# Performance work log

Hardware: AMD Instinct MI355X
Metric: run time of the kernel (lower is better)

Reference implementation:

```python
import jax, jax.numpy as jnp
import numpy as np

B, T, C, H = 512, 40, 512, 512


def _gru_dir(x, Wih, Whh, bih, bhh):
    """Single-direction PyTorch-convention GRU. x: [B,T,C] -> [B,T,H]."""
    Hh = Whh.shape[1]
    # precompute input projections for all timesteps: [B,T,3H]
    gx = jnp.einsum('btc,gc->btg', x, Wih) + bih

    def step(h, gxt):
        gh = h @ Whh.T + bhh  # [B,3H]
        r = jax.nn.sigmoid(gxt[:, :Hh] + gh[:, :Hh])
        z = jax.nn.sigmoid(gxt[:, Hh:2 * Hh] + gh[:, Hh:2 * Hh])
        n = jnp.tanh(gxt[:, 2 * Hh:] + r * gh[:, 2 * Hh:])
        h_new = (1.0 - z) * n + z * h
        return h_new, h_new

    h0 = jnp.zeros((x.shape[0], Hh), x.dtype)
    _, ys = jax.lax.scan(step, h0, jnp.swapaxes(gx, 0, 1))  # [T,B,H]
    return jnp.swapaxes(ys, 0, 1)


def setup_inputs() -> dict:
    key = jax.random.key(0)
    ks = jax.random.split(key, 10)
    s = 1.0 / np.sqrt(H)  # PyTorch default init scale
    lengths = jax.random.randint(ks[0], (B,), 5, T + 1)
    valid = jnp.arange(T)[None, :] < lengths[:, None]  # [B,T]
    ref_expr = jax.random.normal(ks[1], (B, T, C), jnp.float32) * valid[..., None]
    mk = lambda k, shape: jax.random.uniform(k, shape, jnp.float32, -s, s)
    return {
        'ref_expr': ref_expr,
        'Wih_f': mk(ks[2], (3 * H, C)), 'Whh_f': mk(ks[3], (3 * H, H)),
        'bih_f': mk(ks[4], (3 * H,)), 'bhh_f': mk(ks[5], (3 * H,)),
        'Wih_b': mk(ks[6], (3 * H, C)), 'Whh_b': mk(ks[7], (3 * H, H)),
        'bih_b': mk(ks[8], (3 * H,)), 'bhh_b': mk(ks[9], (3 * H,)),
    }


def reference(ref_expr, Wih_f, Whh_f, bih_f, bhh_f, Wih_b, Whh_b, bih_b, bhh_b):
    # padded positions are all-zero embedding vectors -> masked out
    valid = jnp.any(ref_expr != 0, axis=-1)  # [B,T], True = keep
    y_fwd = _gru_dir(ref_expr, Wih_f, Whh_f, bih_f, bhh_f)
    y_bwd = _gru_dir(ref_expr[:, ::-1], Wih_b, Whh_b, bih_b, bhh_b)[:, ::-1]
    y_word = jnp.concatenate([y_fwd, y_bwd], axis=-1)  # [B,T,2H]
    # masked max pooling over valid tokens (output_type='max')
    neg = jnp.finfo(y_word.dtype).min
    y = jnp.max(jnp.where(valid[..., None], y_word, neg), axis=1, keepdims=True)
    return y  # [B,1,2H]
```

## Files before the change

kernel.cpp:

```cpp
#include <hip/hip_runtime.h>
#include <hip/hip_bf16.h>
#include <float.h>

#define BB 512
#define TT 40
#define CC 512
#define HH 512

typedef short bf16x8 __attribute__((ext_vector_type(8)));
typedef float f32x4 __attribute__((ext_vector_type(4)));
typedef unsigned short ushortx8 __attribute__((ext_vector_type(8)));

__device__ __forceinline__ unsigned short f2bf(float f){
  union { float f; unsigned int i; } v; v.f = f;
  unsigned int r = v.i + 0x7fffu + ((v.i >> 16) & 1u);
  return (unsigned short)(r >> 16);
}

__device__ __forceinline__ bf16x8 load_sc0(const unsigned short* p){
  bf16x8 r;
  asm volatile("global_load_dwordx4 %0, %1, off sc0" : "=v"(r) : "v"(p));
  return r;
}
#define WAITV(N) do { asm volatile("s_waitcnt vmcnt(" #N ")" ::: "memory"); \
                      __builtin_amdgcn_sched_barrier(0); } while(0)

__device__ __forceinline__ float fast_sigmoid(float x){
  return __builtin_amdgcn_rcpf(1.f + __expf(-x));
}
__device__ __forceinline__ float fast_tanh(float x){
  return 1.f - 2.f*__builtin_amdgcn_rcpf(__expf(2.f*x) + 1.f);
}

__global__ void prep_x_kernel(const float* __restrict__ x, unsigned short* __restrict__ xb,
                              float* __restrict__ maskT){
  int w = blockIdx.x*4 + (threadIdx.x>>6);
  int lane = threadIdx.x & 63;
  const float* src = x + (size_t)w*CC + lane*8;
  f32x4 a = *(const f32x4*)(src);
  f32x4 b = *(const f32x4*)(src+4);
  ushortx8 o;
  o[0]=f2bf(a[0]); o[1]=f2bf(a[1]); o[2]=f2bf(a[2]); o[3]=f2bf(a[3]);
  o[4]=f2bf(b[0]); o[5]=f2bf(b[1]); o[6]=f2bf(b[2]); o[7]=f2bf(b[3]);
  *(ushortx8*)(xb + (size_t)w*CC + lane*8) = o;
  bool nz = (a[0]!=0.f)||(a[1]!=0.f)||(a[2]!=0.f)||(a[3]!=0.f)||
            (b[0]!=0.f)||(b[1]!=0.f)||(b[2]!=0.f)||(b[3]!=0.f);
  unsigned long long bal = __ballot(nz);
  if (lane==0){
    int b_ = w / TT, t_ = w % TT;
    maskT[t_*BB + b_] = bal ? 1.0f : 0.0f;
  }
}

__global__ void cvt_kernel(const float* __restrict__ src, unsigned short* __restrict__ dst, int n){
  int i = blockIdx.x*blockDim.x + threadIdx.x;
  if (i < n) dst[i] = f2bf(src[i]);
}

__global__ void init_h_kernel(unsigned short* __restrict__ hb, unsigned int* __restrict__ ctr){
  int i = blockIdx.x*blockDim.x + threadIdx.x;
  hb[i] = 0;
  if (i < 8) ctr[i*32] = 0u;
}

__global__ __launch_bounds__(256) void gru_persist_kernel(
    const unsigned short* __restrict__ xb,
    const unsigned short* __restrict__ wihF, const unsigned short* __restrict__ whhF,
    const unsigned short* __restrict__ wihB, const unsigned short* __restrict__ whhB,
    const float* __restrict__ bihF, const float* __restrict__ bhhF,
    const float* __restrict__ bihB, const float* __restrict__ bhhB,
    const float* __restrict__ maskT,
    unsigned short* __restrict__ hb,
    float* __restrict__ out, unsigned int* __restrict__ ctr)
{
  const int bid   = blockIdx.x;
  const int grp   = bid & 7;
  const int strip = bid >> 3;
  const int dir   = grp >> 2;
  const int bslab = grp & 3;
  const int b0 = bslab * 128;
  const int n0 = strip * 16;
  unsigned int* myctr = ctr + grp*32;

  const unsigned short* wih = dir ? wihB : wihF;
  const unsigned short* whh = dir ? whhB : whhF;
  const float* bih = dir ? bihB : bihF;
  const float* bhh = dir ? bhhB : bhhF;

  const int tid  = threadIdx.x;
  const int lane = tid & 63;
  const int lr   = lane & 15;
  const int lkg  = lane >> 4;
  const int wv   = tid >> 6;
  const int wrow = wv * 32;

  __shared__ __align__(16) unsigned short wlds[48 * 1024];
  for (int q = tid; q < 6144; q += 256) {
    const int row = q >> 7;
    const int kc  = (q & 127) * 8;
    const int g   = row >> 4;
    const int c   = row & 15;
    const unsigned short* src =
        (kc < 512 ? wih : whh) + ((size_t)(g*HH + n0 + c))*512 + (kc & 511);
    const int kb = kc * 2;
    *(ushortx8*)((char*)wlds + row*2048 + (kb ^ ((row & 7) << 4))) =
        *(const ushortx8*)src;
  }
  __syncthreads();

  const int jj = n0 + lr;
  const float br  = bih[jj]        + bhh[jj];
  const float bz  = bih[HH + jj]   + bhh[HH + jj];
  const float bnx = bih[2*HH + jj];
  const float bnh = bhh[2*HH + jj];

  float omax[2][4], hreg[2][4];
  #pragma unroll
  for (int mf=0; mf<2; ++mf)
    #pragma unroll
    for (int j=0; j<4; ++j){ omax[mf][j] = -FLT_MAX; hreg[mf][j] = 0.f; }

  const int swz = (lr & 7) << 4;
  const char* wbase = (const char*)wlds + lr*2048;

  for (int t = 0; t < TT; ++t) {
    const int tx = dir ? (TT-1-t) : t;
    const int bi = t & 1;
    const unsigned short* hbin = hb + (size_t)(dir*2 + bi)      * (BB*HH);
    unsigned short* hbout      = hb + (size_t)(dir*2 + (bi^1))  * (BB*HH);

    f32x4 ar[2], az[2], anx[2], anh[2];
    #pragma unroll
    for (int mf=0; mf<2; ++mf){ ar[mf]=0.f; az[mf]=0.f; anx[mf]=0.f; anh[mf]=0.f; }

    const unsigned short* xr0 = xb + ((size_t)(b0 + wrow + lr     )*TT + tx)*CC;
    const unsigned short* xr1 = xb + ((size_t)(b0 + wrow + 16 + lr)*TT + tx)*CC;

    #pragma unroll
    for (int kk = 0; kk < 16; ++kk) {
      const int ko = kk*32 + lkg*8;
      bf16x8 a0 = *(const bf16x8*)(xr0 + ko);
      bf16x8 a1 = *(const bf16x8*)(xr1 + ko);
      const int kbx = (ko*2) ^ swz;
      bf16x8 brf = *(const bf16x8*)(wbase +         kbx);
      bf16x8 bzf = *(const bf16x8*)(wbase + 32768 + kbx);
      bf16x8 bnf = *(const bf16x8*)(wbase + 65536 + kbx);
      ar[0]  = __builtin_amdgcn_mfma_f32_16x16x32_bf16(a0, brf, ar[0],0,0,0);
      ar[1]  = __builtin_amdgcn_mfma_f32_16x16x32_bf16(a1, brf, ar[1],0,0,0);
      az[0]  = __builtin_amdgcn_mfma_f32_16x16x32_bf16(a0, bzf, az[0],0,0,0);
      az[1]  = __builtin_amdgcn_mfma_f32_16x16x32_bf16(a1, bzf, az[1],0,0,0);
      anx[0] = __builtin_amdgcn_mfma_f32_16x16x32_bf16(a0, bnf, anx[0],0,0,0);
      anx[1] = __builtin_amdgcn_mfma_f32_16x16x32_bf16(a1, bnf, anx[1],0,0,0);
    }

    const float* mrow = maskT + tx*BB + b0 + wrow + lkg*4;
    const f32x4 mk0 = *(const f32x4*)(mrow);
    const f32x4 mk1 = *(const f32x4*)(mrow + 16);

    if (t > 0) {
      const unsigned int tgt = 128u*(unsigned)t;
      unsigned int spin = 0;
      while (__hip_atomic_load(myctr, __ATOMIC_RELAXED, __HIP_MEMORY_SCOPE_AGENT) < tgt
             && ++spin < (1u<<24))
        __builtin_amdgcn_s_sleep(1);
    }

    WAITV(0);

    const unsigned short* hr0 = hbin + (size_t)(b0 + wrow + lr     )*HH;
    const unsigned short* hr1 = hbin + (size_t)(b0 + wrow + 16 + lr)*HH;
    bf16x8 c0 = load_sc0(hr0 + lkg*8);
    bf16x8 c1 = load_sc0(hr1 + lkg*8);
    #pragma unroll
    for (int kk = 0; kk < 16; ++kk) {
      const int ko = kk*32 + lkg*8;
      bf16x8 p0, p1;
      if (kk < 15) { p0 = load_sc0(hr0 + ko + 32); p1 = load_sc0(hr1 + ko + 32); }
      const int kbx = (1024 + ko*2) ^ swz;
      bf16x8 brf = *(const bf16x8*)(wbase +         kbx);
      bf16x8 bzf = *(const bf16x8*)(wbase + 32768 + kbx);
      bf16x8 bnf = *(const bf16x8*)(wbase + 65536 + kbx);
      if (kk < 15) { WAITV(2); } else { WAITV(0); }
      ar[0]  = __builtin_amdgcn_mfma_f32_16x16x32_bf16(c0, brf, ar[0],0,0,0);
      ar[1]  = __builtin_amdgcn_mfma_f32_16x16x32_bf16(c1, brf, ar[1],0,0,0);
      az[0]  = __builtin_amdgcn_mfma_f32_16x16x32_bf16(c0, bzf, az[0],0,0,0);
      az[1]  = __builtin_amdgcn_mfma_f32_16x16x32_bf16(c1, bzf, az[1],0,0,0);
      anh[0] = __builtin_amdgcn_mfma_f32_16x16x32_bf16(c0, bnf, anh[0],0,0,0);
      anh[1] = __builtin_amdgcn_mfma_f32_16x16x32_bf16(c1, bnf, anh[1],0,0,0);
      if (kk < 15) { c0 = p0; c1 = p1; }
    }

    #pragma unroll
    for (int mf=0; mf<2; ++mf){
      const f32x4 mk = mf ? mk1 : mk0;
      #pragma unroll
      for (int j=0; j<4; ++j){
        const int m = wrow + mf*16 + lkg*4 + j;
        const int b = b0 + m;
        const float rg = fast_sigmoid(ar[mf][j] + br);
        const float zg = fast_sigmoid(az[mf][j] + bz);
        const float ng = fast_tanh(anx[mf][j] + bnx + rg*(anh[mf][j] + bnh));
        const float hn = (1.f - zg)*ng + zg*hreg[mf][j];
        hreg[mf][j] = hn;
        hbout[(size_t)b*HH + jj] = f2bf(hn);
        const float cand = (mk[j] != 0.f) ? hn : -FLT_MAX;
        omax[mf][j] = fmaxf(omax[mf][j], cand);
      }
    }

    if (t < TT-1) {
      WAITV(0);
      if (lane == 0)
        __hip_atomic_fetch_add(myctr, 1u, __ATOMIC_RELAXED, __HIP_MEMORY_SCOPE_AGENT);
    }
  }

  #pragma unroll
  for (int mf=0; mf<2; ++mf){
    #pragma unroll
    for (int j=0; j<4; ++j){
      const int b = b0 + wrow + mf*16 + lkg*4 + j;
      out[(size_t)b*(2*HH) + dir*HH + jj] = omax[mf][j];
    }
  }
}

extern "C" void kernel_launch(void* const* d_in, const int* in_sizes, int n_in,
                              void* d_out, int out_size, void* d_ws, size_t ws_size,
                              hipStream_t stream) {
  const float* x    = (const float*)d_in[0];
  const float* WihF = (const float*)d_in[1];
  const float* WhhF = (const float*)d_in[2];
  const float* bihF = (const float*)d_in[3];
  const float* bhhF = (const float*)d_in[4];
  const float* WihB = (const float*)d_in[5];
  const float* WhhB = (const float*)d_in[6];
  const float* bihB = (const float*)d_in[7];
  const float* bhhB = (const float*)d_in[8];
  float* out = (float*)d_out;

  char* ws = (char*)d_ws;
  unsigned short* xb    = (unsigned short*)(ws);
  unsigned short* wb    = (unsigned short*)(ws + 20971520);
  unsigned short* wihFb = wb;
  unsigned short* whhFb = wb + 786432;
  unsigned short* wihBb = wb + 2*786432;
  unsigned short* whhBb = wb + 3*786432;
  float* maskT = (float*)(ws + 27262976);
  unsigned short* hb = (unsigned short*)(ws + 27344896);
  unsigned int* ctr  = (unsigned int*)(ws + 29442048);

  prep_x_kernel<<<BB*TT/4, 256, 0, stream>>>(x, xb, maskT);
  cvt_kernel<<<3072, 256, 0, stream>>>(WihF, wihFb, 786432);
  cvt_kernel<<<3072, 256, 0, stream>>>(WhhF, whhFb, 786432);
  cvt_kernel<<<3072, 256, 0, stream>>>(WihB, wihBb, 786432);
  cvt_kernel<<<3072, 256, 0, stream>>>(WhhB, whhBb, 786432);
  init_h_kernel<<<4096, 256, 0, stream>>>(hb, ctr);

  gru_persist_kernel<<<256, 256, 0, stream>>>(xb, wihFb, whhFb, wihBb, whhBb,
                                              bihF, bhhF, bihB, bhhB,
                                              maskT, hb, out, ctr);
}
```

Before: 355.7 us.

## Split GRU block into producer and consumer waves for input and recurrent GEMMs

Each workgroup now has 512 threads. Four producer waves compute the input-projection MFMAs for upcoming timesteps and pass the partial gate accumulators through double-buffered LDS slots, using workgroup-scope flag handshakes. Four consumer waves handle only the recurrent h·Whh GEMM, the gate nonlinearities and the cross-block synchronisation. The goal is to take the x·Wih work off the serial recurrence critical path. The cost is extra LDS traffic, intra-block spin-waits and higher LDS usage (about 148 KB), which must still fit one block per CU.

New measurement: 917.8 us. 158% more time.

```diff
diff --git a/kernel.cpp b/kernel.cpp
--- a/kernel.cpp
+++ b/kernel.cpp
@@ -10,6 +10,11 @@
 typedef short bf16x8 __attribute__((ext_vector_type(8)));
 typedef float f32x4 __attribute__((ext_vector_type(4)));
 typedef unsigned short ushortx8 __attribute__((ext_vector_type(8)));
+
+#define LDSH 49152
+#define LDSA 98304
+#define LDSF 147456
+#define LDSTOT 147968
 
 __device__ __forceinline__ unsigned short f2bf(float f){
   union { float f; unsigned int i; } v; v.f = f;
@@ -63,7 +68,7 @@
   if (i < 8) ctr[i*32] = 0u;
 }
 
-__global__ __launch_bounds__(256) void gru_persist_kernel(
+__global__ __launch_bounds__(512, 2) void gru_persist_kernel(
     const unsigned short* __restrict__ xb,
     const unsigned short* __restrict__ wihF, const unsigned short* __restrict__ whhF,
     const unsigned short* __restrict__ wihB, const unsigned short* __restrict__ whhB,
@@ -92,136 +97,194 @@
   const int lr   = lane & 15;
   const int lkg  = lane >> 4;
   const int wv   = tid >> 6;
-  const int wrow = wv * 32;
-
-  __shared__ __align__(16) unsigned short wlds[48 * 1024];
-  for (int q = tid; q < 6144; q += 256) {
-    const int row = q >> 7;
-    const int kc  = (q & 127) * 8;
-    const int g   = row >> 4;
-    const int c   = row & 15;
+
+  __shared__ __align__(16) char smem[LDSTOT];
+
+  for (int q = tid; q < 6144; q += 512) {
+    const int p_  = q >= 3072;
+    const int r_  = p_ ? (q - 3072) : q;
+    const int row = r_ >> 6;
+    const int kc  = (r_ & 63) * 8;
     const unsigned short* src =
-        (kc < 512 ? wih : whh) + ((size_t)(g*HH + n0 + c))*512 + (kc & 511);
-    const int kb = kc * 2;
-    *(ushortx8*)((char*)wlds + row*2048 + (kb ^ ((row & 7) << 4))) =
+        (p_ ? whh : wih) + ((size_t)((row>>4)*HH + n0 + (row&15)))*512 + kc;
+    *(ushortx8*)(smem + p_*LDSH + row*1024 + ((kc*2) ^ ((row&15)<<4))) =
         *(const ushortx8*)src;
   }
+  if (tid < 4)      *(unsigned int*)(smem + LDSF + tid*16) = 0u;
+  else if (tid < 8) *(unsigned int*)(smem + LDSF + 256 + (tid-4)*16) = 0u;
   __syncthreads();
 
-  const int jj = n0 + lr;
-  const float br  = bih[jj]        + bhh[jj];
-  const float bz  = bih[HH + jj]   + bhh[HH + jj];
-  const float bnx = bih[2*HH + jj];
-  const float bnh = bhh[2*HH + jj];
-
-  float omax[2][4], hreg[2][4];
-  #pragma unroll
-  for (int mf=0; mf<2; ++mf)
+  const int swz = lr << 4;
+
+  if (wv < 4) {
+    const int pair = wv;
+    const int wrow = pair * 32;
+    unsigned int* prod = (unsigned int*)(smem + LDSF + pair*16);
+    unsigned int* cons = (unsigned int*)(smem + LDSF + 256 + pair*16);
+    const char* wb_ = smem + lr*1024;
+
+    for (int t = 0; t < TT; ++t) {
+      const int tx = dir ? (TT-1-t) : t;
+      f32x4 ar[2], az[2], anx[2];
+      #pragma unroll
+      for (int mf=0; mf<2; ++mf){ ar[mf]=0.f; az[mf]=0.f; anx[mf]=0.f; }
+
+      const unsigned short* xr0 = xb + ((size_t)(b0 + wrow + lr     )*TT + tx)*CC;
+      const unsigned short* xr1 = xb + ((size_t)(b0 + wrow + 16 + lr)*TT + tx)*CC;
+
+      #pragma unroll
+      for (int kk = 0; kk < 16; ++kk) {
+        const int ko = kk*32 + lkg*8;
+        bf16x8 a0 = *(const bf16x8*)(xr0 + ko);
+        bf16x8 a1 = *(const bf16x8*)(xr1 + ko);
+        const int kbx = (ko*2) ^ swz;
+        bf16x8 brf = *(const bf16x8*)(wb_ +         kbx);
+        bf16x8 bzf = *(const bf16x8*)(wb_ + 16384 + kbx);
+        bf16x8 bnf = *(const bf16x8*)(wb_ + 32768 + kbx);
+        ar[0]  = __builtin_amdgcn_mfma_f32_16x16x32_bf16(a0, brf, ar[0],0,0,0);
+        ar[1]  = __builtin_amdgcn_mfma_f32_16x16x32_bf16(a1, brf, ar[1],0,0,0);
+        az[0]  = __builtin_amdgcn_mfma_f32_16x16x32_bf16(a0, bzf, az[0],0,0,0);
+        az[1]  = __builtin_amdgcn_mfma_f32_16x16x32_bf16(a1, bzf, az[1],0,0,0);
+        anx[0] = __builtin_amdgcn_mfma_f32_16x16x32_bf16(a0, bnf, anx[0],0,0,0);
+        anx[1] = __builtin_amdgcn_mfma_f32_16x16x32_bf16(a1, bnf, anx[1],0,0,0);
+      }
+
+      if (t >= 2) {
+        const unsigned int tgt = (unsigned)(t-1);
+        unsigned int spin = 0;
+        while (__hip_atomic_load(cons, __ATOMIC_ACQUIRE, __HIP_MEMORY_SCOPE_WORKGROUP) < tgt
+               && ++spin < (1u<<24))
+          __builtin_amdgcn_s_sleep(1);
+      }
+
+      char* slot = smem + LDSA + (pair*2 + (t&1))*6144 + lane*16;
+      *(f32x4*)(slot + 0*1024) = ar[0];
+      *(f32x4*)(slot + 1*1024) = ar[1];
+      *(f32x4*)(slot + 2*1024) = az[0];
+      *(f32x4*)(slot + 3*1024) = az[1];
+      *(f32x4*)(slot + 4*1024) = anx[0];
+      *(f32x4*)(slot + 5*1024) = anx[1];
+      if (lane == 0)
+        __hip_atomic_fetch_add(prod, 1u, __ATOMIC_RELEASE, __HIP_MEMORY_SCOPE_WORKGROUP);
+    }
+  } else {
+    const int pair = wv - 4;
+    const int wrow = pair * 32;
+    unsigned int* prod = (unsigned int*)(smem + LDSF + pair*16);
+    unsigned int* cons = (unsigned int*)(smem + LDSF + 256 + pair*16);
+    const char* wb_ = smem + LDSH + lr*1024;
+
+    const int jj = n0 + lr;
+    const float br  = bih[jj]        + bhh[jj];
+    const float bz  = bih[HH + jj]   + bhh[HH + jj];
+    const float bnx = bih[2*HH + jj];
+    const float bnh = bhh[2*HH + jj];
+
+    float omax[2][4], hreg[2][4];
     #pragma unroll
-    for (int j=0; j<4; ++j){ omax[mf][j] = -FLT_MAX; hreg[mf][j] = 0.f; }
-
-  const int swz = (lr & 7) << 4;
-  const char* wbase = (const char*)wlds + lr*2048;
-
-  for (int t = 0; t < TT; ++t) {
-    const int tx = dir ? (TT-1-t) : t;
-    const int bi = t & 1;
-    const unsigned short* hbin = hb + (size_t)(dir*2 + bi)      * (BB*HH);
-    unsigned short* hbout      = hb + (size_t)(dir*2 + (bi^1))  * (BB*HH);
-
-    f32x4 ar[2], az[2], anx[2], anh[2];
+    for (int mf=0; mf<2; ++mf)
+      #pragma unroll
+      for (int j=0; j<4; ++j){ omax[mf][j] = -FLT_MAX; hreg[mf][j] = 0.f; }
+
+    for (int t = 0; t < TT; ++t) {
+      const int tx = dir ? (TT-1-t) : t;
+      const int bi = t & 1;
+      const unsigned short* hbin = hb + (size_t)(dir*2 + bi)      * (BB*HH);
+      unsigned short* hbout      = hb + (size_t)(dir*2 + (bi^1))  * (BB*HH);
+
+      f32x4 ar[2], az[2], anh[2];
+      #pragma unroll
+      for (int mf=0; mf<2; ++mf){ ar[mf]=0.f; az[mf]=0.f; anh[mf]=0.f; }
+
+      const float* mrow = maskT + tx*BB + b0 + wrow + lkg*4;
+      const f32x4 mk0 = *(const f32x4*)(mrow);
+      const f32x4 mk1 = *(const f32x4*)(mrow + 16);
+
+      if (t > 0) {
+        const unsigned int tgt = 128u*(unsigned)t;
+        unsigned int spin = 0;
+        while (__hip_atomic_load(myctr, __ATOMIC_RELAXED, __HIP_MEMORY_SCOPE_AGENT) < tgt
+               && ++spin < (1u<<24))
+          __builtin_amdgcn_s_sleep(1);
+      }
+      WAITV(0);
+
+      const unsigned short* hr0 = hbin + (size_t)(b0 + wrow + lr     )*HH;
+      const unsigned short* hr1 = hbin + (size_t)(b0 + wrow + 16 + lr)*HH;
+      bf16x8 c0 = load_sc0(hr0 + lkg*8);
+      bf16x8 c1 = load_sc0(hr1 + lkg*8);
+      #pragma unroll
+      for (int kk = 0; kk < 16; ++kk) {
+        const int ko = kk*32 + lkg*8;
+        bf16x8 p0, p1;
+        if (kk < 15) { p0 = load_sc0(hr0 + ko + 32); p1 = load_sc0(hr1 + ko + 32); }
+        const int kbx = (ko*2) ^ swz;
+        bf16x8 brf = *(const bf16x8*)(wb_ +         kbx);
+        bf16x8 bzf = *(const bf16x8*)(wb_ + 16384 + kbx);
+        bf16x8 bnf = *(const bf16x8*)(wb_ + 32768 + kbx);
+        if (kk < 15) { WAITV(2); } else { WAITV(0); }
+        ar[0]  = __builtin_amdgcn_mfma_f32_16x16x32_bf16(c0, brf, ar[0],0,0,0);
+        ar[1]  = __builtin_amdgcn_mfma_f32_16x16x32_bf16(c1, brf, ar[1],0,0,0);
+        az[0]  = __builtin_amdgcn_mfma_f32_16x16x32_bf16(c0, bzf, az[0],0,0,0);
+        az[1]  = __builtin_amdgcn_mfma_f32_16x16x32_bf16(c1, bzf, az[1],0,0,0);
+        anh[0] = __builtin_amdgcn_mfma_f32_16x16x32_bf16(c0, bnf, anh[0],0,0,0);
+        anh[1] = __builtin_amdgcn_mfma_f32_16x16x32_bf16(c1, bnf, anh[1],0,0,0);
+        if (kk < 15) { c0 = p0; c1 = p1; }
+      }
+
+      {
+        unsigned int spin = 0;
+        const unsigned int tgt = (unsigned)(t+1);
+        while (__hip_atomic_load(prod, __ATOMIC_ACQUIRE, __HIP_MEMORY_SCOPE_WORKGROUP) < tgt
+               && ++spin < (1u<<24))
+          __builtin_amdgcn_s_sleep(1);
+      }
+      const char* slot = smem + LDSA + (pair*2 + (t&1))*6144 + lane*16;
+      f32x4 px0 = *(const f32x4*)(slot + 0*1024);
+      f32x4 px1 = *(const f32x4*)(slot + 1*1024);
+      f32x4 pz0 = *(const f32x4*)(slot + 2*1024);
+      f32x4 pz1 = *(const f32x4*)(slot + 3*1024);
+      f32x4 pn0 = *(const f32x4*)(slot + 4*1024);
+      f32x4 pn1 = *(const f32x4*)(slot + 5*1024);
+      asm volatile("s_waitcnt lgkmcnt(0)" ::: "memory");
+      if (lane == 0)
+        __hip_atomic_fetch_add(cons, 1u, __ATOMIC_RELEASE, __HIP_MEMORY_SCOPE_WORKGROUP);
+      ar[0] += px0; ar[1] += px1;
+      az[0] += pz0; az[1] += pz1;
+      const f32x4 anx0 = pn0, anx1 = pn1;
+
+      #pragma unroll
+      for (int mf=0; mf<2; ++mf){
+        const f32x4 mk = mf ? mk1 : mk0;
+        const f32x4 anx_ = mf ? anx1 : anx0;
+        #pragma unroll
+        for (int j=0; j<4; ++j){
+          const int b = b0 + wrow + mf*16 + lkg*4 + j;
+          const float rg = fast_sigmoid(ar[mf][j] + br);
+          const float zg = fast_sigmoid(az[mf][j] + bz);
+          const float ng = fast_tanh(anx_[j] + bnx + rg*(anh[mf][j] + bnh));
+          const float hn = (1.f - zg)*ng + zg*hreg[mf][j];
+          hreg[mf][j] = hn;
+          hbout[(size_t)b*HH + jj] = f2bf(hn);
+          const float cand = (mk[j] != 0.f) ? hn : -FLT_MAX;
+          omax[mf][j] = fmaxf(omax[mf][j], cand);
+        }
+      }
+
+      if (t < TT-1) {
+        WAITV(0);
+        if (lane == 0)
+          __hip_atomic_fetch_add(myctr, 1u, __ATOMIC_RELAXED, __HIP_MEMORY_SCOPE_AGENT);
+      }
+    }
+
     #pragma unroll
-    for (int mf=0; mf<2; ++mf){ ar[mf]=0.f; az[mf]=0.f; anx[mf]=0.f; anh[mf]=0.f; }
-
-    const unsigned short* xr0 = xb + ((size_t)(b0 + wrow + lr     )*TT + tx)*CC;
-    const unsigned short* xr1 = xb + ((size_t)(b0 + wrow + 16 + lr)*TT + tx)*CC;
-
-    #pragma unroll
-    for (int kk = 0; kk < 16; ++kk) {
-      const int ko = kk*32 + lkg*8;
-      bf16x8 a0 = *(const bf16x8*)(xr0 + ko);
-      bf16x8 a1 = *(const bf16x8*)(xr1 + ko);
-      const int kbx = (ko*2) ^ swz;
-      bf16x8 brf = *(const bf16x8*)(wbase +         kbx);
-      bf16x8 bzf = *(const bf16x8*)(wbase + 32768 + kbx);
-      bf16x8 bnf = *(const bf16x8*)(wbase + 65536 + kbx);
-      ar[0]  = __builtin_amdgcn_mfma_f32_16x16x32_bf16(a0, brf, ar[0],0,0,0);
-      ar[1]  = __builtin_amdgcn_mfma_f32_16x16x32_bf16(a1, brf, ar[1],0,0,0);
-      az[0]  = __builtin_amdgcn_mfma_f32_16x16x32_bf16(a0, bzf, az[0],0,0,0);
-      az[1]  = __builtin_amdgcn_mfma_f32_16x16x32_bf16(a1, bzf, az[1],0,0,0);
-      anx[0] = __builtin_amdgcn_mfma_f32_16x16x32_bf16(a0, bnf, anx[0],0,0,0);
-      anx[1] = __builtin_amdgcn_mfma_f32_16x16x32_bf16(a1, bnf, anx[1],0,0,0);
-    }
-
-    const float* mrow = maskT + tx*BB + b0 + wrow + lkg*4;
-    const f32x4 mk0 = *(const f32x4*)(mrow);
-    const f32x4 mk1 = *(const f32x4*)(mrow + 16);
-
-    if (t > 0) {
-      const unsigned int tgt = 128u*(unsigned)t;
-      unsigned int spin = 0;
-      while (__hip_atomic_load(myctr, __ATOMIC_RELAXED, __HIP_MEMORY_SCOPE_AGENT) < tgt
-             && ++spin < (1u<<24))
-        __builtin_amdgcn_s_sleep(1);
-    }
-
-    WAITV(0);
-
-    const unsigned short* hr0 = hbin + (size_t)(b0 + wrow + lr     )*HH;
-    const unsigned short* hr1 = hbin + (size_t)(b0 + wrow + 16 + lr)*HH;
-    bf16x8 c0 = load_sc0(hr0 + lkg*8);
-    bf16x8 c1 = load_sc0(hr1 + lkg*8);
-    #pragma unroll
-    for (int kk = 0; kk < 16; ++kk) {
-      const int ko = kk*32 + lkg*8;
-      bf16x8 p0, p1;
-      if (kk < 15) { p0 = load_sc0(hr0 + ko + 32); p1 = load_sc0(hr1 + ko + 32); }
-      const int kbx = (1024 + ko*2) ^ swz;
-      bf16x8 brf = *(const bf16x8*)(wbase +         kbx);
-      bf16x8 bzf = *(const bf16x8*)(wbase + 32768 + kbx);
-      bf16x8 bnf = *(const bf16x8*)(wbase + 65536 + kbx);
-      if (kk < 15) { WAITV(2); } else { WAITV(0); }
-      ar[0]  = __builtin_amdgcn_mfma_f32_16x16x32_bf16(c0, brf, ar[0],0,0,0);
-      ar[1]  = __builtin_amdgcn_mfma_f32_16x16x32_bf16(c1, brf, ar[1],0,0,0);
-      az[0]  = __builtin_amdgcn_mfma_f32_16x16x32_bf16(c0, bzf, az[0],0,0,0);
-      az[1]  = __builtin_amdgcn_mfma_f32_16x16x32_bf16(c1, bzf, az[1],0,0,0);
-      anh[0] = __builtin_amdgcn_mfma_f32_16x16x32_bf16(c0, bnf, anh[0],0,0,0);
-      anh[1] = __builtin_amdgcn_mfma_f32_16x16x32_bf16(c1, bnf, anh[1],0,0,0);
-      if (kk < 15) { c0 = p0; c1 = p1; }
-    }
-
-    #pragma unroll
-    for (int mf=0; mf<2; ++mf){
-      const f32x4 mk = mf ? mk1 : mk0;
+    for (int mf=0; mf<2; ++mf)
       #pragma unroll
       for (int j=0; j<4; ++j){
-        const int m = wrow + mf*16 + lkg*4 + j;
-        const int b = b0 + m;
-        const float rg = fast_sigmoid(ar[mf][j] + br);
-        const float zg = fast_sigmoid(az[mf][j] + bz);
-        const float ng = fast_tanh(anx[mf][j] + bnx + rg*(anh[mf][j] + bnh));
-        const float hn = (1.f - zg)*ng + zg*hreg[mf][j];
-        hreg[mf][j] = hn;
-        hbout[(size_t)b*HH + jj] = f2bf(hn);
-        const float cand = (mk[j] != 0.f) ? hn : -FLT_MAX;
-        omax[mf][j] = fmaxf(omax[mf][j], cand);
-      }
-    }
-
-    if (t < TT-1) {
-      WAITV(0);
-      if (lane == 0)
-        __hip_atomic_fetch_add(myctr, 1u, __ATOMIC_RELAXED, __HIP_MEMORY_SCOPE_AGENT);
-    }
-  }
-
-  #pragma unroll
-  for (int mf=0; mf<2; ++mf){
-    #pragma unroll
-    for (int j=0; j<4; ++j){
-      const int b = b0 + wrow + mf*16 + lkg*4 + j;
-      out[(size_t)b*(2*HH) + dir*HH + jj] = omax[mf][j];
-    }
+        const int b = b0 + wrow + mf*16 + lkg*4 + j;
+        out[(size_t)b*(2*HH) + dir*HH + (n0 + lr)] = omax[mf][j];
+      }
   }
 }
 
@@ -257,7 +320,7 @@
   cvt_kernel<<<3072, 256, 0, stream>>>(WhhB, whhBb, 786432);
   init_h_kernel<<<4096, 256, 0, stream>>>(hb, ctr);
 
-  gru_persist_kernel<<<256, 256, 0, stream>>>(xb, wihFb, whhFb, wihBb, whhBb,
+  gru_persist_kernel<<<256, 512, 0, stream>>>(xb, wihFb, whhFb, wihBb, whhBb,
                                               bihF, bhhF, bihB, bhhB,
                                               maskT, hb, out, ctr);
 }
```

## Hierarchical block barrier, deeper h prefetch, split LDS layout, vectorized weight convert

Applied to the files above, without the earlier changes.

Each workgroup now gathers its four waves in a shared-memory arrive counter and has a single lane increment the global per-group counter. One lane also polls that global counter and releases the others through an LDS flag, which cuts global atomic traffic and polling contention. The hidden-state loads use a four-deep register prefetch ring instead of double buffering. The weights are split into separate input and hidden LDS halves with a new swizzle, and the bf16 conversion kernels now process 8 elements per thread. The intra-block handoff adds an extra serialization step and uses more registers.

Result: slower. 370.9 us (+4.3%).

```diff
diff --git a/kernel.cpp b/kernel.cpp
--- a/kernel.cpp
+++ b/kernel.cpp
@@ -10,6 +10,10 @@
 typedef short bf16x8 __attribute__((ext_vector_type(8)));
 typedef float f32x4 __attribute__((ext_vector_type(4)));
 typedef unsigned short ushortx8 __attribute__((ext_vector_type(8)));
+
+#define LDSH 49152
+#define LDSF 98304
+#define LDSTOT 98320
 
 __device__ __forceinline__ unsigned short f2bf(float f){
   union { float f; unsigned int i; } v; v.f = f;
@@ -52,9 +56,16 @@
   }
 }
 
-__global__ void cvt_kernel(const float* __restrict__ src, unsigned short* __restrict__ dst, int n){
+__global__ void cvt_kernel(const float* __restrict__ src, unsigned short* __restrict__ dst, int n8){
   int i = blockIdx.x*blockDim.x + threadIdx.x;
-  if (i < n) dst[i] = f2bf(src[i]);
+  if (i < n8){
+    f32x4 a = *(const f32x4*)(src + i*8);
+    f32x4 b = *(const f32x4*)(src + i*8 + 4);
+    ushortx8 o;
+    o[0]=f2bf(a[0]); o[1]=f2bf(a[1]); o[2]=f2bf(a[2]); o[3]=f2bf(a[3]);
+    o[4]=f2bf(b[0]); o[5]=f2bf(b[1]); o[6]=f2bf(b[2]); o[7]=f2bf(b[3]);
+    *(ushortx8*)(dst + i*8) = o;
+  }
 }
 
 __global__ void init_h_kernel(unsigned short* __restrict__ hb, unsigned int* __restrict__ ctr){
@@ -94,18 +105,21 @@
   const int wv   = tid >> 6;
   const int wrow = wv * 32;
 
-  __shared__ __align__(16) unsigned short wlds[48 * 1024];
+  __shared__ __align__(16) char smem[LDSTOT];
+  unsigned int* arrive = (unsigned int*)(smem + LDSF);
+  unsigned int* goflag = (unsigned int*)(smem + LDSF + 8);
+
   for (int q = tid; q < 6144; q += 256) {
-    const int row = q >> 7;
-    const int kc  = (q & 127) * 8;
-    const int g   = row >> 4;
-    const int c   = row & 15;
+    const int p_  = q >= 3072;
+    const int r_  = p_ ? (q - 3072) : q;
+    const int row = r_ >> 6;
+    const int kc  = (r_ & 63) * 8;
     const unsigned short* src =
-        (kc < 512 ? wih : whh) + ((size_t)(g*HH + n0 + c))*512 + (kc & 511);
-    const int kb = kc * 2;
-    *(ushortx8*)((char*)wlds + row*2048 + (kb ^ ((row & 7) << 4))) =
+        (p_ ? whh : wih) + ((size_t)((row>>4)*HH + n0 + (row&15)))*512 + kc;
+    *(ushortx8*)(smem + p_*LDSH + row*1024 + ((kc*2) ^ ((row&15)<<4))) =
         *(const ushortx8*)src;
   }
+  if (tid == 0){ arrive[0] = 0u; goflag[0] = 0u; }
   __syncthreads();
 
   const int jj = n0 + lr;
@@ -120,8 +134,9 @@
     #pragma unroll
     for (int j=0; j<4; ++j){ omax[mf][j] = -FLT_MAX; hreg[mf][j] = 0.f; }
 
-  const int swz = (lr & 7) << 4;
-  const char* wbase = (const char*)wlds + lr*2048;
+  const int swz = lr << 4;
+  const char* wbx = smem + lr*1024;
+  const char* wbh = smem + LDSH + lr*1024;
 
   for (int t = 0; t < TT; ++t) {
     const int tx = dir ? (TT-1-t) : t;
@@ -142,9 +157,9 @@
       bf16x8 a0 = *(const bf16x8*)(xr0 + ko);
       bf16x8 a1 = *(const bf16x8*)(xr1 + ko);
       const int kbx = (ko*2) ^ swz;
-      bf16x8 brf = *(const bf16x8*)(wbase +         kbx);
-      bf16x8 bzf = *(const bf16x8*)(wbase + 32768 + kbx);
-      bf16x8 bnf = *(const bf16x8*)(wbase + 65536 + kbx);
+      bf16x8 brf = *(const bf16x8*)(wbx +         kbx);
+      bf16x8 bzf = *(const bf16x8*)(wbx + 16384 + kbx);
+      bf16x8 bnf = *(const bf16x8*)(wbx + 32768 + kbx);
       ar[0]  = __builtin_amdgcn_mfma_f32_16x16x32_bf16(a0, brf, ar[0],0,0,0);
       ar[1]  = __builtin_amdgcn_mfma_f32_16x16x32_bf16(a1, brf, ar[1],0,0,0);
       az[0]  = __builtin_amdgcn_mfma_f32_16x16x32_bf16(a0, bzf, az[0],0,0,0);
@@ -158,9 +173,16 @@
     const f32x4 mk1 = *(const f32x4*)(mrow + 16);
 
     if (t > 0) {
-      const unsigned int tgt = 128u*(unsigned)t;
+      if (wv == 0 && lane == 0) {
+        const unsigned int tgt = 32u*(unsigned)t;
+        unsigned int spin = 0;
+        while (__hip_atomic_load(myctr, __ATOMIC_RELAXED, __HIP_MEMORY_SCOPE_AGENT) < tgt
+               && ++spin < (1u<<24))
+          __builtin_amdgcn_s_sleep(2);
+        __hip_atomic_store(goflag, (unsigned)t, __ATOMIC_RELEASE, __HIP_MEMORY_SCOPE_WORKGROUP);
+      }
       unsigned int spin = 0;
-      while (__hip_atomic_load(myctr, __ATOMIC_RELAXED, __HIP_MEMORY_SCOPE_AGENT) < tgt
+      while (__hip_atomic_load(goflag, __ATOMIC_ACQUIRE, __HIP_MEMORY_SCOPE_WORKGROUP) < (unsigned)t
              && ++spin < (1u<<24))
         __builtin_amdgcn_s_sleep(1);
     }
@@ -169,25 +191,35 @@
 
     const unsigned short* hr0 = hbin + (size_t)(b0 + wrow + lr     )*HH;
     const unsigned short* hr1 = hbin + (size_t)(b0 + wrow + 16 + lr)*HH;
-    bf16x8 c0 = load_sc0(hr0 + lkg*8);
-    bf16x8 c1 = load_sc0(hr1 + lkg*8);
+    bf16x8 ph[4][2];
+    #pragma unroll
+    for (int q = 0; q < 4; ++q){
+      ph[q][0] = load_sc0(hr0 + q*32 + lkg*8);
+      ph[q][1] = load_sc0(hr1 + q*32 + lkg*8);
+    }
     #pragma unroll
     for (int kk = 0; kk < 16; ++kk) {
       const int ko = kk*32 + lkg*8;
-      bf16x8 p0, p1;
-      if (kk < 15) { p0 = load_sc0(hr0 + ko + 32); p1 = load_sc0(hr1 + ko + 32); }
-      const int kbx = (1024 + ko*2) ^ swz;
-      bf16x8 brf = *(const bf16x8*)(wbase +         kbx);
-      bf16x8 bzf = *(const bf16x8*)(wbase + 32768 + kbx);
-      bf16x8 bnf = *(const bf16x8*)(wbase + 65536 + kbx);
-      if (kk < 15) { WAITV(2); } else { WAITV(0); }
+      const int kbx = (ko*2) ^ swz;
+      bf16x8 brf = *(const bf16x8*)(wbh +         kbx);
+      bf16x8 bzf = *(const bf16x8*)(wbh + 16384 + kbx);
+      bf16x8 bnf = *(const bf16x8*)(wbh + 32768 + kbx);
+      if (kk < 13)      { WAITV(6); }
+      else if (kk == 13){ WAITV(4); }
+      else if (kk == 14){ WAITV(2); }
+      else              { WAITV(0); }
+      bf16x8 c0 = ph[kk&3][0];
+      bf16x8 c1 = ph[kk&3][1];
       ar[0]  = __builtin_amdgcn_mfma_f32_16x16x32_bf16(c0, brf, ar[0],0,0,0);
       ar[1]  = __builtin_amdgcn_mfma_f32_16x16x32_bf16(c1, brf, ar[1],0,0,0);
       az[0]  = __builtin_amdgcn_mfma_f32_16x16x32_bf16(c0, bzf, az[0],0,0,0);
       az[1]  = __builtin_amdgcn_mfma_f32_16x16x32_bf16(c1, bzf, az[1],0,0,0);
       anh[0] = __builtin_amdgcn_mfma_f32_16x16x32_bf16(c0, bnf, anh[0],0,0,0);
       anh[1] = __builtin_amdgcn_mfma_f32_16x16x32_bf16(c1, bnf, anh[1],0,0,0);
-      if (kk < 15) { c0 = p0; c1 = p1; }
+      if (kk < 12) {
+        ph[kk&3][0] = load_sc0(hr0 + (kk+4)*32 + lkg*8);
+        ph[kk&3][1] = load_sc0(hr1 + (kk+4)*32 + lkg*8);
+      }
     }
 
     #pragma unroll
@@ -195,8 +227,7 @@
       const f32x4 mk = mf ? mk1 : mk0;
       #pragma unroll
       for (int j=0; j<4; ++j){
-        const int m = wrow + mf*16 + lkg*4 + j;
-        const int b = b0 + m;
+        const int b = b0 + wrow + mf*16 + lkg*4 + j;
         const float rg = fast_sigmoid(ar[mf][j] + br);
         const float zg = fast_sigmoid(az[mf][j] + bz);
         const float ng = fast_tanh(anx[mf][j] + bnx + rg*(anh[mf][j] + bnh));
@@ -211,18 +242,25 @@
     if (t < TT-1) {
       WAITV(0);
       if (lane == 0)
+        __hip_atomic_fetch_add(arrive, 1u, __ATOMIC_RELEASE, __HIP_MEMORY_SCOPE_WORKGROUP);
+      if (wv == 0 && lane == 0) {
+        const unsigned int tgt = 4u*(unsigned)(t+1);
+        unsigned int spin = 0;
+        while (__hip_atomic_load(arrive, __ATOMIC_ACQUIRE, __HIP_MEMORY_SCOPE_WORKGROUP) < tgt
+               && ++spin < (1u<<24))
+          __builtin_amdgcn_s_sleep(1);
         __hip_atomic_fetch_add(myctr, 1u, __ATOMIC_RELAXED, __HIP_MEMORY_SCOPE_AGENT);
+      }
     }
   }
 
   #pragma unroll
-  for (int mf=0; mf<2; ++mf){
+  for (int mf=0; mf<2; ++mf)
     #pragma unroll
     for (int j=0; j<4; ++j){
       const int b = b0 + wrow + mf*16 + lkg*4 + j;
       out[(size_t)b*(2*HH) + dir*HH + jj] = omax[mf][j];
     }
-  }
 }
 
 extern "C" void kernel_launch(void* const* d_in, const int* in_sizes, int n_in,
@@ -251,10 +289,10 @@
   unsigned int* ctr  = (unsigned int*)(ws + 29442048);
 
   prep_x_kernel<<<BB*TT/4, 256, 0, stream>>>(x, xb, maskT);
-  cvt_kernel<<<3072, 256, 0, stream>>>(WihF, wihFb, 786432);
-  cvt_kernel<<<3072, 256, 0, stream>>>(WhhF, whhFb, 786432);
-  cvt_kernel<<<3072, 256, 0, stream>>>(WihB, wihBb, 786432);
-  cvt_kernel<<<3072, 256, 0, stream>>>(WhhB, whhBb, 786432);
+  cvt_kernel<<<384, 256, 0, stream>>>(WihF, wihFb, 98304);
+  cvt_kernel<<<384, 256, 0, stream>>>(WhhF, whhFb, 98304);
+  cvt_kernel<<<384, 256, 0, stream>>>(WihB, wihBb, 98304);
+  cvt_kernel<<<384, 256, 0, stream>>>(WhhB, whhBb, 98304);
   init_h_kernel<<<4096, 256, 0, stream>>>(hb, ctr);
 
   gru_persist_kernel<<<256, 256, 0, stream>>>(xb, wihFb, whhFb, wihBb, whhBb,
```
